# Optimization experiments

Measured on AMD Instinct MI355X. Metric: run time of the kernel, lower is better.

Reference implementation:

```python
import jax, jax.numpy as jnp
import numpy as np

B, S, D_MODEL, H, D = 2, 2048, 1024, 16, 64
SCALE = 1.0 / float(np.sqrt(D))


def setup_inputs() -> dict:
    key = jax.random.key(0)
    ks = jax.random.split(key, 5)
    x = jax.random.normal(ks[0], (B, S, D_MODEL), jnp.float32)
    qkv_w = jax.random.normal(ks[1], (3 * H * D, D_MODEL), jnp.float32) * 0.02
    out_w = jax.random.normal(ks[2], (D_MODEL, H * D), jnp.float32) * 0.02
    bias_p = jax.random.uniform(ks[3], (H, 1, 1), jnp.float32) * 2.0  # torch.rand(...)*2
    bias_a = jax.random.uniform(ks[4], (H, 1, 1), jnp.float32)
    # standard geometric RoPE frequencies over d_head//2 = 32 channels
    rope_freqs = 10000.0 ** (-jnp.arange(D // 2, dtype=jnp.float32) / (D // 2))
    return {"x": x, "qkv_w": qkv_w, "out_w": out_w,
            "bias_p": bias_p, "bias_a": bias_a, "rope_freqs": rope_freqs}


def _rope(t, c, s):
    # t: [B,H,S,d]; c,s: [1,1,S,d/2]. Split-half rotation as in apply_rope.
    d2 = t.shape[-1] // 2
    t1, t2 = t[..., :d2], t[..., d2:]
    return jnp.concatenate([t1 * c - t2 * s, t1 * s + t2 * c], axis=-1)


def reference(x, qkv_w, out_w, bias_p, bias_a, rope_freqs):
    Bb, Ss, _ = x.shape
    qkv = (x @ qkv_w.T).reshape(Bb, Ss, 3, H, D)
    q = qkv[:, :, 0].transpose(0, 2, 1, 3)  # [B,H,S,d]
    k = qkv[:, :, 1].transpose(0, 2, 1, 3)
    v = qkv[:, :, 2].transpose(0, 2, 1, 3)
    pos = jnp.arange(Ss, dtype=jnp.float32)
    ang = pos[:, None] * rope_freqs[None, :]                 # [S, d/2]
    c = jnp.cos(ang)[None, None]
    s = jnp.sin(ang)[None, None]
    q = _rope(q, c, s)
    k = _rope(k, c, s)
    scores = jnp.einsum('bhqd,bhkd->bhqk', q, k) * SCALE     # [B,H,S,S]
    p = jnp.maximum(bias_p, 0.01)                            # clamp(min=0.01)
    a = jnp.maximum(bias_a, 0.01)
    dist = jnp.abs(pos[None, :] - pos[:, None])              # [S,S]
    kb = -p * jnp.log1p(a * dist)                            # [H,S,S]
    attn = jax.nn.softmax(scores + kb[None], axis=-1)
    out = jnp.einsum('bhqk,bhkd->bhqd', attn, v)             # [B,H,S,d]
    out = out.transpose(0, 2, 1, 3).reshape(Bb, Ss, H * D)
    return out @ out_w.T
```

## Files before the change

### kernel.cpp

```cpp
#include <hip/hip_runtime.h>
#include <math.h>

#define BATCH  2
#define SEQ    2048
#define DMODEL 1024
#define NH     16
#define HD     64
#define NQKV   3072
#define ROWS   (BATCH*SEQ)
#define QSCALE 0.18033688f

typedef unsigned short u16;
typedef unsigned int   u32;
typedef __bf16 bf16x8 __attribute__((ext_vector_type(8)));
typedef float  f32x4  __attribute__((ext_vector_type(4)));

typedef const __attribute__((address_space(1))) void* gptr_t;
typedef __attribute__((address_space(3))) void* lptr_t;

__device__ __forceinline__ void gload16(lptr_t l, const void* g) {
    __builtin_amdgcn_global_load_lds((gptr_t)g, l, 16, 0, 0);
}

__device__ __forceinline__ u16 f2bf(float f) {
    unsigned int u = __float_as_uint(f);
    u += 0x7FFFu + ((u >> 16) & 1u);
    return (u16)(u >> 16);
}
__device__ __forceinline__ float bf2f(u16 v) {
    return __uint_as_float(((unsigned int)v) << 16);
}
__device__ __forceinline__ u32 pk2(float lo, float hi) {
#if __has_builtin(__builtin_amdgcn_cvt_pk_bf16_f32)
    typedef __bf16 bf16x2 __attribute__((ext_vector_type(2)));
    union { bf16x2 v; u32 u; } cv;
    cv.v = __builtin_amdgcn_cvt_pk_bf16_f32(lo, hi);
    return cv.u;
#else
    return (u32)f2bf(lo) | ((u32)f2bf(hi) << 16);
#endif
}
__device__ __forceinline__ float fexp2(float x) {
#if __has_builtin(__builtin_amdgcn_exp2f)
    return __builtin_amdgcn_exp2f(x);
#else
    return exp2f(x);
#endif
}

__global__ void f2bf3_kernel(const float* __restrict__ a, int na,
                             const float* __restrict__ b, int nb,
                             const float* __restrict__ c, int nc,
                             u16* __restrict__ oa, u16* __restrict__ ob,
                             u16* __restrict__ oc)
{
    int i = (blockIdx.x * 256 + threadIdx.x) * 4;
    const float* s; u16* d; int base;
    if (i < na)                { s = a; d = oa; base = i; }
    else if (i < na + nb)      { s = b; d = ob; base = i - na; }
    else if (i < na + nb + nc) { s = c; d = oc; base = i - na - nb; }
    else return;
    float4 v = *(const float4*)(s + base);
    u16 o[4] = { f2bf(v.x), f2bf(v.y), f2bf(v.z), f2bf(v.w) };
    *(uint2*)(d + base) = *(const uint2*)o;
}

__global__ void wtab_kernel(const float* __restrict__ bias_p,
                            const float* __restrict__ bias_a,
                            float* __restrict__ wtab)
{
    int idx = blockIdx.x * 256 + threadIdx.x;
    int h = idx >> 11;
    int d = idx & (SEQ - 1);
    float p = fmaxf(bias_p[h], 0.01f);
    float a = fmaxf(bias_a[h], 0.01f);
    wtab[idx] = __expf(-p * log1pf(a * (float)d));
}

__global__ void rope_table_kernel(const float* __restrict__ freqs, float* __restrict__ tab)
{
    int idx = blockIdx.x * 256 + threadIdx.x;
    int s = idx >> 5, d = idx & 31;
    float sn, cs;
    sincosf((float)s * freqs[d], &sn, &cs);
    tab[idx * 2]     = cs;
    tab[idx * 2 + 1] = sn;
}

template<bool BF16OUT>
__global__ __launch_bounds__(256) void gemm_bf16(
    const u16* __restrict__ A, const u16* __restrict__ B,
    void* __restrict__ Cout, int M, int N, int K)
{
    __shared__ __align__(16) u16 As[128][32];
    __shared__ __align__(16) u16 Bs[128][32];
    const int tid  = threadIdx.x;
    const int wave = tid >> 6, lane = tid & 63;
    const int quad = lane >> 4, l16 = lane & 15;
    const int wrow = (wave >> 1) * 64, wcol = (wave & 1) * 64;
    const int bm = blockIdx.x * 128, bn = blockIdx.y * 128;

    const int srow = lane >> 2;
    const int scol = ((lane & 3) ^ (srow & 3)) * 8;
    const int fsw = (quad ^ (l16 & 3)) * 8;

    f32x4 acc[4][4];
#pragma unroll
    for (int i = 0; i < 4; ++i)
#pragma unroll
        for (int j = 0; j < 4; ++j) acc[i][j] = (f32x4){0.f,0.f,0.f,0.f};

    const u16* Ag0 = A + (size_t)(bm + wave*32 + srow)      * K + scol;
    const u16* Ag1 = A + (size_t)(bm + wave*32 + 16 + srow) * K + scol;
    const u16* Bg0 = B + (size_t)(bn + wave*32 + srow)      * K + scol;
    const u16* Bg1 = B + (size_t)(bn + wave*32 + 16 + srow) * K + scol;

    for (int k0 = 0; k0 < K; k0 += 32) {
        __syncthreads();
        gload16((lptr_t)&As[wave*32][0],      Ag0 + k0);
        gload16((lptr_t)&As[wave*32 + 16][0], Ag1 + k0);
        gload16((lptr_t)&Bs[wave*32][0],      Bg0 + k0);
        gload16((lptr_t)&Bs[wave*32 + 16][0], Bg1 + k0);
        __syncthreads();
        bf16x8 af[4], bfr[4];
#pragma unroll
        for (int i = 0; i < 4; ++i)
            af[i] = *(const bf16x8*)&As[wrow + i*16 + l16][fsw];
#pragma unroll
        for (int j = 0; j < 4; ++j)
            bfr[j] = *(const bf16x8*)&Bs[wcol + j*16 + l16][fsw];
#pragma unroll
        for (int i = 0; i < 4; ++i)
#pragma unroll
            for (int j = 0; j < 4; ++j)
                acc[i][j] = __builtin_amdgcn_mfma_f32_16x16x32_bf16(af[i], bfr[j], acc[i][j], 0, 0, 0);
    }

#pragma unroll
    for (int i = 0; i < 4; ++i)
#pragma unroll
        for (int j = 0; j < 4; ++j) {
            int col = bn + wcol + j*16 + l16;
#pragma unroll
            for (int r = 0; r < 4; ++r) {
                int row = bm + wrow + i*16 + quad*4 + r;
                if (BF16OUT) ((u16*)Cout)[(size_t)row * N + col] = f2bf(acc[i][j][r]);
                else         ((float*)Cout)[(size_t)row * N + col] = acc[i][j][r];
            }
        }
}

__global__ __launch_bounds__(256) void qkv_convert(
    const u16* __restrict__ qkv_bf, const float* __restrict__ cs_tab,
    u16* __restrict__ Qb, u16* __restrict__ Kb, u16* __restrict__ Vt)
{
    __shared__ __align__(16) u16 Vtile[64][72];
    const int tid = threadIdx.x;
    const int r = tid >> 2, c = tid & 3;
    const int s0 = blockIdx.x * 64, h = blockIdx.y, b = blockIdx.z;
    const int s = s0 + r;
    const u16* src = qkv_bf + (size_t)(b * SEQ + s) * NQKV + h * HD;
    const size_t hb = (size_t)(b * NH + h) * SEQ * HD;

    *(uint4*)&Vtile[r][c*16]     = *(const uint4*)(src + 2*NH*HD + c*16);
    *(uint4*)&Vtile[r][c*16 + 8] = *(const uint4*)(src + 2*NH*HD + c*16 + 8);

    {
        const u16* m = src + ((c < 2) ? 0 : NH*HD);
        const int d1 = (c & 1) * 16;
        u16 x1[16], x2[16];
        *(uint4*)&x1[0] = *(const uint4*)(m + d1);
        *(uint4*)&x1[8] = *(const uint4*)(m + d1 + 8);
        *(uint4*)&x2[0] = *(const uint4*)(m + d1 + 32);
        *(uint4*)&x2[8] = *(const uint4*)(m + d1 + 40);
        const float* ct = cs_tab + ((size_t)s * 32 + d1) * 2;
        const float sc = (c < 2) ? QSCALE : 1.0f;
        u16 y1[16], y2[16];
#pragma unroll
        for (int u = 0; u < 16; ++u) {
            float cs = ct[u*2], sn = ct[u*2 + 1];
            float a = bf2f(x1[u]), bq = bf2f(x2[u]);
            y1[u] = f2bf((a * cs - bq * sn) * sc);
            y2[u] = f2bf((a * sn + bq * cs) * sc);
        }
        u16* dst = ((c < 2) ? Qb : Kb) + hb + (size_t)s * HD + d1;
        *(uint4*)(dst)      = *(const uint4*)&y1[0];
        *(uint4*)(dst + 8)  = *(const uint4*)&y1[8];
        *(uint4*)(dst + 32) = *(const uint4*)&y2[0];
        *(uint4*)(dst + 40) = *(const uint4*)&y2[8];
    }
    __syncthreads();

    u16 vv[16];
#pragma unroll
    for (int u = 0; u < 16; ++u) vv[u] = Vtile[c*16 + u][r];
    u16* dst = Vt + hb + (size_t)r * SEQ + s0 + c*16;
    *(uint4*)(dst)     = *(const uint4*)&vv[0];
    *(uint4*)(dst + 8) = *(const uint4*)&vv[8];
}

__global__ __launch_bounds__(256) void attn_mfma(
    const u16* __restrict__ Qb, const u16* __restrict__ Kb,
    const u16* __restrict__ Vt, const float* __restrict__ wtab,
    u16* __restrict__ attn_bf)
{
    __shared__ __align__(16) u16 Ks[64*64];
    __shared__ __align__(16) u16 Vs[64*64];
    __shared__ __align__(16) u16 Ps[64][72];
    __shared__ u32 ws2[128];
    __shared__ float lred[4][64];
    __shared__ float linv[64];

    const int tid = threadIdx.x;
    const int wave = tid >> 6, lane = tid & 63;
    const int quad = lane >> 4, l16 = lane & 15;
    const int q0 = blockIdx.x * 64, h = blockIdx.y, b = blockIdx.z;

    const u16* Qh = Qb + (size_t)(b * NH + h) * SEQ * HD;
    const u16* Kh = Kb + (size_t)(b * NH + h) * SEQ * HD;
    const u16* Vh = Vt + (size_t)(b * NH + h) * HD * SEQ;
    const float* wh = wtab + h * SEQ;

    bf16x8 qf0[4], qf1[4];
#pragma unroll
    for (int qj = 0; qj < 4; ++qj) {
        const u16* qr = Qh + (size_t)(q0 + qj*16 + l16) * HD + quad * 8;
        qf0[qj] = *(const bf16x8*)qr;
        qf1[qj] = *(const bf16x8*)(qr + 32);
    }

    const int srow = lane >> 3;
    const int scol = ((lane & 7) ^ srow) * 8;
    const u16* Kg0 = Kh + (size_t)(wave*16 + srow)     * HD + scol;
    const u16* Kg1 = Kh + (size_t)(wave*16 + 8 + srow) * HD + scol;
    const u16* Vg0 = Vh + (size_t)(wave*16 + srow)     * SEQ + scol;
    const u16* Vg1 = Vh + (size_t)(wave*16 + 8 + srow) * SEQ + scol;

    const int sw  = (quad ^ (l16 & 7)) * 8;
    const int mb0 = 63 + l16 - wave*16 - quad*4 - 3;

    float l_p[4] = {0.f, 0.f, 0.f, 0.f};
    f32x4 o[4];
#pragma unroll
    for (int j = 0; j < 4; ++j) o[j] = (f32x4){0.f,0.f,0.f,0.f};

    for (int kt = 0; kt < SEQ / 64; ++kt) {
        const int k0 = kt * 64;
        __syncthreads();
        gload16((lptr_t)&Ks[(wave*16)*64],     Kg0 + (size_t)k0 * HD);
        gload16((lptr_t)&Ks[(wave*16 + 8)*64], Kg1 + (size_t)k0 * HD);
        gload16((lptr_t)&Vs[(wave*16)*64],     Vg0 + k0);
        gload16((lptr_t)&Vs[(wave*16 + 8)*64], Vg1 + k0);
        if (tid < 128) {
            int i0 = (q0 - k0 - 63) + tid;
            int a0 = i0 < 0 ? -i0 : i0;  if (a0 > SEQ-1) a0 = SEQ-1;
            int i1 = i0 + 1;
            int a1 = i1 < 0 ? -i1 : i1;  if (a1 > SEQ-1) a1 = SEQ-1;
            ws2[tid] = pk2(wh[a0], wh[a1]);
        }
        __syncthreads();

        bf16x8 kf0 = *(const bf16x8*)&Ks[(wave*16 + l16)*64 + sw];
        bf16x8 kf1 = *(const bf16x8*)&Ks[(wave*16 + l16)*64 + (sw ^ 32)];
#pragma unroll
        for (int qj = 0; qj < 4; ++qj) {
            f32x4 z = (f32x4){0.f,0.f,0.f,0.f};
            z = __builtin_amdgcn_mfma_f32_16x16x32_bf16(kf0, qf0[qj], z, 0, 0, 0);
            z = __builtin_amdgcn_mfma_f32_16x16x32_bf16(kf1, qf1[qj], z, 0, 0, 0);
            const int mbase = mb0 + qj*16;
            u32 pA = ws2[mbase], pB = ws2[mbase + 2];
            float w3 = __uint_as_float(pA << 16);
            float w2 = __uint_as_float(pA & 0xffff0000u);
            float w1 = __uint_as_float(pB << 16);
            float w0 = __uint_as_float(pB & 0xffff0000u);
            float e0 = fexp2(z[0]) * w0, e1 = fexp2(z[1]) * w1;
            float e2 = fexp2(z[2]) * w2, e3 = fexp2(z[3]) * w3;
            l_p[qj] += (e0 + e1) + (e2 + e3);
            *(uint2*)&Ps[qj*16 + l16][wave*16 + quad*4] =
                make_uint2(pk2(e0, e1), pk2(e2, e3));
        }
        __syncthreads();

        bf16x8 pf0 = *(const bf16x8*)&Ps[wave*16 + l16][quad*8];
        bf16x8 pf1 = *(const bf16x8*)&Ps[wave*16 + l16][32 + quad*8];
#pragma unroll
        for (int j = 0; j < 4; ++j) {
            bf16x8 vf0 = *(const bf16x8*)&Vs[(j*16 + l16)*64 + sw];
            bf16x8 vf1 = *(const bf16x8*)&Vs[(j*16 + l16)*64 + (sw ^ 32)];
            o[j] = __builtin_amdgcn_mfma_f32_16x16x32_bf16(pf0, vf0, o[j], 0, 0, 0);
            o[j] = __builtin_amdgcn_mfma_f32_16x16x32_bf16(pf1, vf1, o[j], 0, 0, 0);
        }
    }

#pragma unroll
    for (int qj = 0; qj < 4; ++qj) {
        float l = l_p[qj];
        l += __shfl_xor(l, 16);
        l += __shfl_xor(l, 32);
        if (quad == 0) lred[wave][qj*16 + l16] = l;
    }
    __syncthreads();
    if (tid < 64)
        linv[tid] = 1.0f / (lred[0][tid] + lred[1][tid] + lred[2][tid] + lred[3][tid]);
    __syncthreads();
#pragma unroll
    for (int r = 0; r < 4; ++r) {
        const int q = wave*16 + quad*4 + r;
        float inv = linv[q];
        u16* dst = attn_bf + (size_t)(b * SEQ + q0 + q) * DMODEL + h * HD;
#pragma unroll
        for (int j = 0; j < 4; ++j)
            dst[j*16 + l16] = f2bf(o[j][r] * inv);
    }
}

extern "C" void kernel_launch(void* const* d_in, const int* in_sizes, int n_in,
                              void* d_out, int out_size, void* d_ws, size_t ws_size,
                              hipStream_t stream)
{
    (void)in_sizes; (void)n_in; (void)out_size; (void)ws_size;
    const float* x      = (const float*)d_in[0];
    const float* qkv_w  = (const float*)d_in[1];
    const float* out_w  = (const float*)d_in[2];
    const float* bias_p = (const float*)d_in[3];
    const float* bias_a = (const float*)d_in[4];
    const float* freqs  = (const float*)d_in[5];
    float* out = (float*)d_out;

    char* ws = (char*)d_ws;
    u16*   qkv_bf  = (u16*)ws;
    u16*   attn_bf = (u16*)ws;
    u16*   x_bf    = (u16*)(ws + 25165824);
    u16*   Qb      = x_bf;
    u16*   w1_bf   = (u16*)(ws + 33554432);
    u16*   w2_bf   = (u16*)(ws + 39845888);
    u16*   Kb      = (u16*)(ws + 41943040);
    u16*   Vt      = (u16*)(ws + 50331648);
    float* wtab    = (float*)(ws + 58720256);
    float* cs_tab  = (float*)(ws + 58720256 + 131072);

    const int na = ROWS*DMODEL, nb = NQKV*DMODEL, nc = DMODEL*DMODEL;
    f2bf3_kernel<<<dim3((na+nb+nc)/1024), 256, 0, stream>>>(x, na, qkv_w, nb, out_w, nc,
                                                            x_bf, w1_bf, w2_bf);
    rope_table_kernel<<<dim3(SEQ*32/256), 256, 0, stream>>>(freqs, cs_tab);
    wtab_kernel<<<dim3(NH*SEQ/256), 256, 0, stream>>>(bias_p, bias_a, wtab);

    gemm_bf16<true><<<dim3(ROWS/128, NQKV/128), 256, 0, stream>>>(x_bf, w1_bf, qkv_bf, ROWS, NQKV, DMODEL);
    qkv_convert<<<dim3(SEQ/64, NH, BATCH), 256, 0, stream>>>(qkv_bf, cs_tab, Qb, Kb, Vt);
    attn_mfma<<<dim3(SEQ/64, NH, BATCH), 256, 0, stream>>>(Qb, Kb, Vt, wtab, attn_bf);
    gemm_bf16<false><<<dim3(ROWS/128, DMODEL/128), 256, 0, stream>>>(attn_bf, w2_bf, out, ROWS, DMODEL, DMODEL);
}
```

Measured before the change: 234.1 us.

## Fuse RoPE and QKV split into GEMM epilogue; load K/V directly in attention

```diff
diff --git a/kernel.cpp b/kernel.cpp
--- a/kernel.cpp
+++ b/kernel.cpp
@@ -87,11 +87,12 @@
     tab[idx * 2 + 1] = sn;
 }
 
-template<bool BF16OUT>
-__global__ __launch_bounds__(256) void gemm_bf16(
+__global__ __launch_bounds__(256) void gemm_qkv(
     const u16* __restrict__ A, const u16* __restrict__ B,
-    void* __restrict__ Cout, int M, int N, int K)
-{
+    const float* __restrict__ cs_tab,
+    u16* __restrict__ Qb, u16* __restrict__ Kb, u16* __restrict__ Vt)
+{
+    const int M = ROWS, N = NQKV, K = DMODEL;
     __shared__ __align__(16) u16 As[128][32];
     __shared__ __align__(16) u16 Bs[128][32];
     const int tid  = threadIdx.x;
@@ -136,6 +137,95 @@
                 acc[i][j] = __builtin_amdgcn_mfma_f32_16x16x32_bf16(af[i], bfr[j], acc[i][j], 0, 0, 0);
     }
 
+    const int tcol = (bn + wcol) >> 6;
+    const int t = tcol >> 4, h = tcol & 15;
+    const int bq = bm >> 11;
+    const int sb = (bm & (SEQ - 1)) + wrow;
+    const size_t hb = (size_t)(bq * NH + h) * SEQ * HD;
+
+    if (t == 2) {
+#pragma unroll
+        for (int i = 0; i < 4; ++i) {
+            const int s = sb + i*16 + quad*4;
+#pragma unroll
+            for (int j = 0; j < 4; ++j) {
+                const int d = j*16 + l16;
+                uint2 pv = make_uint2(pk2(acc[i][j][0], acc[i][j][1]),
+                                      pk2(acc[i][j][2], acc[i][j][3]));
+                *(uint2*)&Vt[hb + (size_t)d * SEQ + s] = pv;
+            }
+        }
+    } else {
+        const float sc = (t == 0) ? QSCALE : 1.0f;
+        u16* dstb = ((t == 0) ? Qb : Kb) + hb;
+#pragma unroll
+        for (int i = 0; i < 4; ++i) {
+#pragma unroll
+            for (int r = 0; r < 4; ++r) {
+                const int s = sb + i*16 + quad*4 + r;
+                const float2* ct = (const float2*)(cs_tab + ((size_t)s * 32 + l16) * 2);
+                float2 cs0 = ct[0];
+                float2 cs1 = ct[16];
+                float a0 = acc[i][0][r], a1 = acc[i][1][r];
+                float a2 = acc[i][2][r], a3 = acc[i][3][r];
+                u16* dst = dstb + (size_t)s * HD;
+                dst[l16]      = f2bf((a0*cs0.x - a2*cs0.y) * sc);
+                dst[16 + l16] = f2bf((a1*cs1.x - a3*cs1.y) * sc);
+                dst[32 + l16] = f2bf((a0*cs0.y + a2*cs0.x) * sc);
+                dst[48 + l16] = f2bf((a1*cs1.y + a3*cs1.x) * sc);
+            }
+        }
+    }
+}
+
+__global__ __launch_bounds__(256) void gemm_out(
+    const u16* __restrict__ A, const u16* __restrict__ B,
+    float* __restrict__ Cout, int M, int N, int K)
+{
+    __shared__ __align__(16) u16 As[128][32];
+    __shared__ __align__(16) u16 Bs[128][32];
+    const int tid  = threadIdx.x;
+    const int wave = tid >> 6, lane = tid & 63;
+    const int quad = lane >> 4, l16 = lane & 15;
+    const int wrow = (wave >> 1) * 64, wcol = (wave & 1) * 64;
+    const int bm = blockIdx.x * 128, bn = blockIdx.y * 128;
+
+    const int srow = lane >> 2;
+    const int scol = ((lane & 3) ^ (srow & 3)) * 8;
+    const int fsw = (quad ^ (l16 & 3)) * 8;
+
+    f32x4 acc[4][4];
+#pragma unroll
+    for (int i = 0; i < 4; ++i)
+#pragma unroll
+        for (int j = 0; j < 4; ++j) acc[i][j] = (f32x4){0.f,0.f,0.f,0.f};
+
+    const u16* Ag0 = A + (size_t)(bm + wave*32 + srow)      * K + scol;
+    const u16* Ag1 = A + (size_t)(bm + wave*32 + 16 + srow) * K + scol;
+    const u16* Bg0 = B + (size_t)(bn + wave*32 + srow)      * K + scol;
+    const u16* Bg1 = B + (size_t)(bn + wave*32 + 16 + srow) * K + scol;
+
+    for (int k0 = 0; k0 < K; k0 += 32) {
+        __syncthreads();
+        gload16((lptr_t)&As[wave*32][0],      Ag0 + k0);
+        gload16((lptr_t)&As[wave*32 + 16][0], Ag1 + k0);
+        gload16((lptr_t)&Bs[wave*32][0],      Bg0 + k0);
+        gload16((lptr_t)&Bs[wave*32 + 16][0], Bg1 + k0);
+        __syncthreads();
+        bf16x8 af[4], bfr[4];
+#pragma unroll
+        for (int i = 0; i < 4; ++i)
+            af[i] = *(const bf16x8*)&As[wrow + i*16 + l16][fsw];
+#pragma unroll
+        for (int j = 0; j < 4; ++j)
+            bfr[j] = *(const bf16x8*)&Bs[wcol + j*16 + l16][fsw];
+#pragma unroll
+        for (int i = 0; i < 4; ++i)
+#pragma unroll
+            for (int j = 0; j < 4; ++j)
+                acc[i][j] = __builtin_amdgcn_mfma_f32_16x16x32_bf16(af[i], bfr[j], acc[i][j], 0, 0, 0);
+    }
+
 #pragma unroll
     for (int i = 0; i < 4; ++i)
 #pragma unroll
@@ -144,59 +234,9 @@
 #pragma unroll
             for (int r = 0; r < 4; ++r) {
                 int row = bm + wrow + i*16 + quad*4 + r;
-                if (BF16OUT) ((u16*)Cout)[(size_t)row * N + col] = f2bf(acc[i][j][r]);
-                else         ((float*)Cout)[(size_t)row * N + col] = acc[i][j][r];
+                Cout[(size_t)row * N + col] = acc[i][j][r];
             }
         }
-}
-
-__global__ __launch_bounds__(256) void qkv_convert(
-    const u16* __restrict__ qkv_bf, const float* __restrict__ cs_tab,
-    u16* __restrict__ Qb, u16* __restrict__ Kb, u16* __restrict__ Vt)
-{
-    __shared__ __align__(16) u16 Vtile[64][72];
-    const int tid = threadIdx.x;
-    const int r = tid >> 2, c = tid & 3;
-    const int s0 = blockIdx.x * 64, h = blockIdx.y, b = blockIdx.z;
-    const int s = s0 + r;
-    const u16* src = qkv_bf + (size_t)(b * SEQ + s) * NQKV + h * HD;
-    const size_t hb = (size_t)(b * NH + h) * SEQ * HD;
-
-    *(uint4*)&Vtile[r][c*16]     = *(const uint4*)(src + 2*NH*HD + c*16);
-    *(uint4*)&Vtile[r][c*16 + 8] = *(const uint4*)(src + 2*NH*HD + c*16 + 8);
-
-    {
-        const u16* m = src + ((c < 2) ? 0 : NH*HD);
-        const int d1 = (c & 1) * 16;
-        u16 x1[16], x2[16];
-        *(uint4*)&x1[0] = *(const uint4*)(m + d1);
-        *(uint4*)&x1[8] = *(const uint4*)(m + d1 + 8);
-        *(uint4*)&x2[0] = *(const uint4*)(m + d1 + 32);
-        *(uint4*)&x2[8] = *(const uint4*)(m + d1 + 40);
-        const float* ct = cs_tab + ((size_t)s * 32 + d1) * 2;
-        const float sc = (c < 2) ? QSCALE : 1.0f;
-        u16 y1[16], y2[16];
-#pragma unroll
-        for (int u = 0; u < 16; ++u) {
-            float cs = ct[u*2], sn = ct[u*2 + 1];
-            float a = bf2f(x1[u]), bq = bf2f(x2[u]);
-            y1[u] = f2bf((a * cs - bq * sn) * sc);
-            y2[u] = f2bf((a * sn + bq * cs) * sc);
-        }
-        u16* dst = ((c < 2) ? Qb : Kb) + hb + (size_t)s * HD + d1;
-        *(uint4*)(dst)      = *(const uint4*)&y1[0];
-        *(uint4*)(dst + 8)  = *(const uint4*)&y1[8];
-        *(uint4*)(dst + 32) = *(const uint4*)&y2[0];
-        *(uint4*)(dst + 40) = *(const uint4*)&y2[8];
-    }
-    __syncthreads();
-
-    u16 vv[16];
-#pragma unroll
-    for (int u = 0; u < 16; ++u) vv[u] = Vtile[c*16 + u][r];
-    u16* dst = Vt + hb + (size_t)r * SEQ + s0 + c*16;
-    *(uint4*)(dst)     = *(const uint4*)&vv[0];
-    *(uint4*)(dst + 8) = *(const uint4*)&vv[8];
 }
 
 __global__ __launch_bounds__(256) void attn_mfma(
@@ -204,10 +244,8 @@
     const u16* __restrict__ Vt, const float* __restrict__ wtab,
     u16* __restrict__ attn_bf)
 {
-    __shared__ __align__(16) u16 Ks[64*64];
-    __shared__ __align__(16) u16 Vs[64*64];
     __shared__ __align__(16) u16 Ps[64][72];
-    __shared__ u32 ws2[128];
+    __shared__ u32 ws2[4][128];
     __shared__ float lred[4][64];
     __shared__ float linv[64];
 
@@ -229,14 +267,7 @@
         qf1[qj] = *(const bf16x8*)(qr + 32);
     }
 
-    const int srow = lane >> 3;
-    const int scol = ((lane & 7) ^ srow) * 8;
-    const u16* Kg0 = Kh + (size_t)(wave*16 + srow)     * HD + scol;
-    const u16* Kg1 = Kh + (size_t)(wave*16 + 8 + srow) * HD + scol;
-    const u16* Vg0 = Vh + (size_t)(wave*16 + srow)     * SEQ + scol;
-    const u16* Vg1 = Vh + (size_t)(wave*16 + 8 + srow) * SEQ + scol;
-
-    const int sw  = (quad ^ (l16 & 7)) * 8;
+    const u16* kptr = Kh + (size_t)(wave*16 + l16) * HD + quad * 8;
     const int mb0 = 63 + l16 - wave*16 - quad*4 - 3;
 
     float l_p[4] = {0.f, 0.f, 0.f, 0.f};
@@ -247,28 +278,34 @@
     for (int kt = 0; kt < SEQ / 64; ++kt) {
         const int k0 = kt * 64;
         __syncthreads();
-        gload16((lptr_t)&Ks[(wave*16)*64],     Kg0 + (size_t)k0 * HD);
-        gload16((lptr_t)&Ks[(wave*16 + 8)*64], Kg1 + (size_t)k0 * HD);
-        gload16((lptr_t)&Vs[(wave*16)*64],     Vg0 + k0);
-        gload16((lptr_t)&Vs[(wave*16 + 8)*64], Vg1 + k0);
-        if (tid < 128) {
-            int i0 = (q0 - k0 - 63) + tid;
+
+#pragma unroll
+        for (int u0 = 0; u0 < 2; ++u0) {
+            int u = lane + u0*64;
+            int i0 = (q0 - k0 - 63) + u;
             int a0 = i0 < 0 ? -i0 : i0;  if (a0 > SEQ-1) a0 = SEQ-1;
             int i1 = i0 + 1;
             int a1 = i1 < 0 ? -i1 : i1;  if (a1 > SEQ-1) a1 = SEQ-1;
-            ws2[tid] = pk2(wh[a0], wh[a1]);
-        }
-        __syncthreads();
-
-        bf16x8 kf0 = *(const bf16x8*)&Ks[(wave*16 + l16)*64 + sw];
-        bf16x8 kf1 = *(const bf16x8*)&Ks[(wave*16 + l16)*64 + (sw ^ 32)];
+            ws2[wave][u] = pk2(wh[a0], wh[a1]);
+        }
+
+        bf16x8 kf0 = *(const bf16x8*)(kptr + (size_t)k0 * HD);
+        bf16x8 kf1 = *(const bf16x8*)(kptr + (size_t)k0 * HD + 32);
+        bf16x8 vf0[4], vf1[4];
+#pragma unroll
+        for (int j = 0; j < 4; ++j) {
+            const u16* vp = Vh + (size_t)(j*16 + l16) * SEQ + k0 + quad * 8;
+            vf0[j] = *(const bf16x8*)vp;
+            vf1[j] = *(const bf16x8*)(vp + 32);
+        }
+
 #pragma unroll
         for (int qj = 0; qj < 4; ++qj) {
             f32x4 z = (f32x4){0.f,0.f,0.f,0.f};
             z = __builtin_amdgcn_mfma_f32_16x16x32_bf16(kf0, qf0[qj], z, 0, 0, 0);
             z = __builtin_amdgcn_mfma_f32_16x16x32_bf16(kf1, qf1[qj], z, 0, 0, 0);
             const int mbase = mb0 + qj*16;
-            u32 pA = ws2[mbase], pB = ws2[mbase + 2];
+            u32 pA = ws2[wave][mbase], pB = ws2[wave][mbase + 2];
             float w3 = __uint_as_float(pA << 16);
             float w2 = __uint_as_float(pA & 0xffff0000u);
             float w1 = __uint_as_float(pB << 16);
@@ -285,10 +322,8 @@
         bf16x8 pf1 = *(const bf16x8*)&Ps[wave*16 + l16][32 + quad*8];
 #pragma unroll
         for (int j = 0; j < 4; ++j) {
-            bf16x8 vf0 = *(const bf16x8*)&Vs[(j*16 + l16)*64 + sw];
-            bf16x8 vf1 = *(const bf16x8*)&Vs[(j*16 + l16)*64 + (sw ^ 32)];
-            o[j] = __builtin_amdgcn_mfma_f32_16x16x32_bf16(pf0, vf0, o[j], 0, 0, 0);
-            o[j] = __builtin_amdgcn_mfma_f32_16x16x32_bf16(pf1, vf1, o[j], 0, 0, 0);
+            o[j] = __builtin_amdgcn_mfma_f32_16x16x32_bf16(pf0, vf0[j], o[j], 0, 0, 0);
+            o[j] = __builtin_amdgcn_mfma_f32_16x16x32_bf16(pf1, vf1[j], o[j], 0, 0, 0);
         }
     }
 
@@ -328,10 +363,9 @@
     float* out = (float*)d_out;
 
     char* ws = (char*)d_ws;
-    u16*   qkv_bf  = (u16*)ws;
     u16*   attn_bf = (u16*)ws;
+    u16*   Qb      = (u16*)(ws + 8388608);
     u16*   x_bf    = (u16*)(ws + 25165824);
-    u16*   Qb      = x_bf;
     u16*   w1_bf   = (u16*)(ws + 33554432);
     u16*   w2_bf   = (u16*)(ws + 39845888);
     u16*   Kb      = (u16*)(ws + 41943040);
@@ -345,8 +379,7 @@
     rope_table_kernel<<<dim3(SEQ*32/256), 256, 0, stream>>>(freqs, cs_tab);
     wtab_kernel<<<dim3(NH*SEQ/256), 256, 0, stream>>>(bias_p, bias_a, wtab);
 
-    gemm_bf16<true><<<dim3(ROWS/128, NQKV/128), 256, 0, stream>>>(x_bf, w1_bf, qkv_bf, ROWS, NQKV, DMODEL);
-    qkv_convert<<<dim3(SEQ/64, NH, BATCH), 256, 0, stream>>>(qkv_bf, cs_tab, Qb, Kb, Vt);
+    gemm_qkv<<<dim3(ROWS/128, NQKV/128), 256, 0, stream>>>(x_bf, w1_bf, cs_tab, Qb, Kb, Vt);
     attn_mfma<<<dim3(SEQ/64, NH, BATCH), 256, 0, stream>>>(Qb, Kb, Vt, wtab, attn_bf);
-    gemm_bf16<false><<<dim3(ROWS/128, DMODEL/128), 256, 0, stream>>>(attn_bf, w2_bf, out, ROWS, DMODEL, DMODEL);
-}
+    gemm_out<<<dim3(ROWS/128, DMODEL/128), 256, 0, stream>>>(attn_bf, w2_bf, out, ROWS, DMODEL, DMODEL);
+}
```

New measurement: 325.1 us. +38.9%, slower.
